# Performance work log

Measured on AMD Instinct MI355X. Metric: run time of the kernel, lower is better.

Reference implementation:

```python
import jax, jax.numpy as jnp
import numpy as np

B, S, HID = 1, 2048, 4096
NH, NKV, HD = 32, 8, 128
GROUPS = NH // NKV
SCALING = HD ** -0.5


def approx_matmul(a, b):
    # BaselineApproxMatmulFP16: matmul performed in fp16 precision
    return jnp.matmul(a.astype(jnp.float16), b.astype(jnp.float16)).astype(a.dtype)


def rotate_half(x):
    x1, x2 = jnp.split(x, 2, axis=-1)
    return jnp.concatenate([-x2, x1], axis=-1)


def setup_inputs() -> dict:
    key = jax.random.key(0)
    ks = jax.random.split(key, 6)
    hidden_states = jax.random.normal(ks[0], (B, S, HID), jnp.float32)
    # Proper RoPE tables (HF llama convention: freqs duplicated across halves)
    inv_freq = 1.0 / (10000.0 ** (jnp.arange(0, HD, 2, dtype=jnp.float32) / HD))
    t = jnp.arange(S, dtype=jnp.float32)
    freqs = jnp.outer(t, inv_freq)                      # [S, HD/2]
    emb = jnp.concatenate([freqs, freqs], axis=-1)      # [S, HD]
    cos = jnp.cos(emb)[None]                            # [B, S, HD]
    sin = jnp.sin(emb)[None]
    # Additive causal mask [B,1,S,S]
    causal = jnp.triu(jnp.full((S, S), -1e9, jnp.float32), k=1)[None, None]
    scale = 0.02
    wq = jax.random.normal(ks[1], (HID, NH * HD), jnp.float32) * scale
    wk = jax.random.normal(ks[2], (HID, NKV * HD), jnp.float32) * scale
    wv = jax.random.normal(ks[3], (HID, NKV * HD), jnp.float32) * scale
    wo = jax.random.normal(ks[4], (NH * HD, HID), jnp.float32) * scale
    return {"hidden_states": hidden_states, "cos": cos, "sin": sin,
            "attn_mask": causal, "wq": wq, "wk": wk, "wv": wv, "wo": wo}


def reference(hidden_states, cos, sin, attn_mask, wq, wk, wv, wo):
    x = hidden_states
    # projections -> [B, heads, S, HD]
    q = (x @ wq).reshape(B, S, NH, HD).transpose(0, 2, 1, 3)
    k = (x @ wk).reshape(B, S, NKV, HD).transpose(0, 2, 1, 3)
    v = (x @ wv).reshape(B, S, NKV, HD).transpose(0, 2, 1, 3)
    # RoPE
    c = cos[:, None]  # [B,1,S,HD]
    s = sin[:, None]
    q = q * c + rotate_half(q) * s
    k = k * c + rotate_half(k) * s
    # repeat_kv (GQA): [B,NKV,S,HD] -> [B,NH,S,HD]
    k = jnp.repeat(k, GROUPS, axis=1)
    v = jnp.repeat(v, GROUPS, axis=1)
    # eager attention with fp16 approx matmul
    attn = approx_matmul(q, k.transpose(0, 1, 3, 2)) * SCALING  # [B,NH,S,S]
    attn = attn + attn_mask
    attn = jax.nn.softmax(attn.astype(jnp.float32), axis=-1).astype(q.dtype)
    out = approx_matmul(attn, v)                                # [B,NH,S,HD]
    out = out.transpose(0, 2, 1, 3).reshape(B, S, NH * HD)
    return out @ wo
```

## Files before the change

kernel.cpp:

```cpp
#include <hip/hip_runtime.h>
#include <hip/hip_bf16.h>
#include <hip/hip_fp16.h>

typedef _Float16 half8 __attribute__((ext_vector_type(8)));
typedef _Float16 half4 __attribute__((ext_vector_type(4)));
typedef float f32x4 __attribute__((ext_vector_type(4)));
typedef unsigned int u32;

#define S_LEN 2048
#define HID_DIM 4096
#define N_HEADS 32
#define N_KV 8
#define HEAD_DIM 128
#define SCALE_QK 0.08838834764831845f

__device__ __forceinline__ void async16(void* lds, const void* gptr) {
  __builtin_amdgcn_global_load_lds(
      (const __attribute__((address_space(1))) u32*)gptr,
      (__attribute__((address_space(3))) u32*)lds, 16, 0, 0);
}

__device__ __forceinline__ void transpose_tile(const float* __restrict__ src,
                                               _Float16* __restrict__ dst, int R, int C,
                                               int bx, int by, float (*tile)[73], int t) {
  {
    const int c4 = (t & 15) * 4;
    const int r0 = t >> 4;
#pragma unroll
    for (int i = 0; i < 4; i++) {
      int r = r0 + 16 * i;
      float4 v = *(const float4*)&src[(long)(by * 64 + r) * C + bx * 64 + c4];
      tile[r][c4] = v.x; tile[r][c4 + 1] = v.y; tile[r][c4 + 2] = v.z; tile[r][c4 + 3] = v.w;
    }
  }
  __syncthreads();
  const int kc = t & 7;
  const int n0 = t >> 3;
#pragma unroll
  for (int p = 0; p < 2; p++) {
    int n = n0 + 32 * p;
    half8 o;
#pragma unroll
    for (int j = 0; j < 8; j++) o[j] = (_Float16)tile[kc * 8 + j][n];
    *(half8*)&dst[(long)(bx * 64 + n) * R + by * 64 + kc * 8] = o;
  }
}

__global__ void prep_kernel(const float* __restrict__ x, _Float16* __restrict__ Xh,
                            const float* __restrict__ wq, _Float16* __restrict__ WqT,
                            const float* __restrict__ wk, const float* __restrict__ wv,
                            _Float16* __restrict__ WkvT) {
  __shared__ float tile[64][73];
  const int bid = blockIdx.x;
  const int t = threadIdx.x;
  if (bid < 4096) {
    int i = bid * 256 + t;
    float4 a = ((const float4*)x)[2 * i];
    float4 b = ((const float4*)x)[2 * i + 1];
    half8 h;
    h[0] = (_Float16)a.x; h[1] = (_Float16)a.y; h[2] = (_Float16)a.z; h[3] = (_Float16)a.w;
    h[4] = (_Float16)b.x; h[5] = (_Float16)b.y; h[6] = (_Float16)b.z; h[7] = (_Float16)b.w;
    ((half8*)Xh)[i] = h;
  } else if (bid < 8192) {
    int tt = bid - 4096;
    transpose_tile(wq, WqT, 4096, 4096, tt & 63, tt >> 6, tile, t);
  } else if (bid < 9216) {
    int tt = bid - 8192;
    transpose_tile(wk, WkvT, 4096, 1024, tt & 15, tt >> 4, tile, t);
  } else {
    int tt = bid - 9216;
    transpose_tile(wv, WkvT + (size_t)1024 * 4096, 4096, 1024, tt & 15, tt >> 4, tile, t);
  }
}

__global__ __launch_bounds__(256, 3) void gemm_qkv(
    const _Float16* __restrict__ A, const _Float16* __restrict__ BtQ,
    const _Float16* __restrict__ BtKV, _Float16* __restrict__ Qt,
    _Float16* __restrict__ Kt, _Float16* __restrict__ Vt,
    const float* __restrict__ cosb, const float* __restrict__ sinb) {
  __shared__ __align__(16) char smem[34816];
  _Float16* As = (_Float16*)smem;
  _Float16* Bs = (_Float16*)(smem + 16384);
  const int K = 4096;
  const int tid = threadIdx.x, lane = tid & 63, wid = tid >> 6;
  const int row0 = blockIdx.y * 128;
  const int col0 = blockIdx.x * 128;
  const int wm = wid >> 1, wn = wid & 1;
  const int lr = lane & 15, lg = lane >> 4;

  const _Float16* bbase = (col0 < 4096) ? (BtQ + (long)col0 * K)
                                        : (BtKV + (long)(col0 - 4096) * K);
  const int scol = ((lane & 7) ^ ((lane >> 3) & 7)) * 8;
  const _Float16* aptr = A + (long)(row0 + wid * 32 + (lane >> 3)) * K + scol;
  const _Float16* bptr = bbase + (long)(wid * 32 + (lane >> 3)) * K + scol;
  _Float16* alds = As + (wid * 4) * 512;
  _Float16* blds = Bs + (wid * 4) * 512;

  f32x4 acc[4][4] = {};
  for (int k0 = 0; k0 < K; k0 += 64) {
#pragma unroll
    for (int j = 0; j < 4; j++) {
      async16(alds + j * 512, aptr + k0 + (long)j * 8 * K);
      async16(blds + j * 512, bptr + k0 + (long)j * 8 * K);
    }
    __syncthreads();
    half8 a[2][4], b[2][4];
#pragma unroll
    for (int kk = 0; kk < 2; kk++)
#pragma unroll
      for (int mf = 0; mf < 4; mf++) {
        a[kk][mf] = *(const half8*)&As[(wm * 64 + mf * 16 + lr) * 64 +
                                       (((kk * 4 + lg) ^ (lr & 7)) * 8)];
        b[kk][mf] = *(const half8*)&Bs[(wn * 64 + mf * 16 + lr) * 64 +
                                       (((kk * 4 + lg) ^ (lr & 7)) * 8)];
      }
#pragma unroll
    for (int kk = 0; kk < 2; kk++)
#pragma unroll
      for (int mf = 0; mf < 4; mf++)
#pragma unroll
        for (int nf = 0; nf < 4; nf++)
          acc[mf][nf] =
              __builtin_amdgcn_mfma_f32_16x16x32_f16(a[kk][mf], b[kk][nf], acc[mf][nf], 0, 0, 0);
    __syncthreads();
  }

  if (col0 < 4096) {
#pragma unroll
    for (int mf = 0; mf < 4; mf++)
#pragma unroll
      for (int nf = 0; nf < 4; nf++) {
        int rbase = row0 + wm * 64 + mf * 16 + lg * 4;
        int col = col0 + wn * 64 + nf * 16 + lr;
        int h = col >> 7, d = col & 127;
        long off = ((long)((h * 128 + (rbase >> 4)) * 4 + (d >> 5))) * 512 +
                   ((d >> 3) & 3) * 128 + (rbase & 15) * 8 + (d & 7);
#pragma unroll
        for (int i = 0; i < 4; i++) Qt[off + i * 8] = (_Float16)acc[mf][nf][i];
      }
  } else if (col0 < 5120) {
    const int g = (col0 - 4096) >> 7;
    float* fl = (float*)smem;
    if (wn == 1) {
#pragma unroll
      for (int mf = 0; mf < 4; mf++)
#pragma unroll
        for (int nf = 0; nf < 4; nf++)
#pragma unroll
          for (int i = 0; i < 4; i++)
            fl[(wm * 64 + mf * 16 + lg * 4 + i) * 68 + nf * 16 + lr] = acc[mf][nf][i];
    }
    __syncthreads();
    if (wn == 0) {
#pragma unroll
      for (int mf = 0; mf < 4; mf++)
#pragma unroll
        for (int nf = 0; nf < 4; nf++)
#pragma unroll
          for (int i = 0; i < 4; i++) {
            int s_local = wm * 64 + mf * 16 + lg * 4 + i;
            int d = nf * 16 + lr;
            int s_glob = row0 + s_local;
            float lo = acc[mf][nf][i];
            float hi = fl[s_local * 68 + d];
            float c = cosb[s_glob * 128 + d];
            float sn = sinb[s_glob * 128 + d];
            long off = ((long)((g * 128 + (s_glob >> 4)) * 4 + (d >> 5))) * 512 +
                       ((d >> 3) & 3) * 128 + (s_glob & 15) * 8 + (d & 7);
            Kt[off] = (_Float16)(lo * c - hi * sn);
            Kt[off + 1024] = (_Float16)(hi * c + lo * sn);
          }
    }
  } else {
#pragma unroll
    for (int mf = 0; mf < 4; mf++)
#pragma unroll
      for (int nf = 0; nf < 4; nf++) {
        int rbase = row0 + wm * 64 + mf * 16 + lg * 4;
        int col = col0 + wn * 64 + nf * 16 + lr;
        int gc = col - 5120;
        int gq = gc >> 7, d = gc & 127;
        int dt = d >> 4, lrr = d & 15;
        int kvb = rbase >> 5, lgv = (rbase >> 3) & 3, j = rbase & 7;
        half4 v;
#pragma unroll
        for (int i = 0; i < 4; i++) v[i] = (_Float16)acc[mf][nf][i];
        long off = ((long)(gq * 64 + kvb) * 8 + dt) * 512 + (lgv * 16 + lrr) * 8 + j;
        *(half4*)&Vt[off] = v;
      }
  }
}

__global__ __launch_bounds__(256, 3) void gemm_out(
    const _Float16* __restrict__ A, const _Float16* __restrict__ Bt,
    float* __restrict__ C) {
  __shared__ _Float16 As[128 * 64];
  __shared__ _Float16 Bs[128 * 64];
  const int K = 4096;
  const int tid = threadIdx.x, lane = tid & 63, wid = tid >> 6;
  const int row0 = blockIdx.y * 128;
  const int col0 = blockIdx.x * 128;
  const int wm = wid >> 1, wn = wid & 1;
  const int lr = lane & 15, lg = lane >> 4;

  const int scol = ((lane & 7) ^ ((lane >> 3) & 7)) * 8;
  const _Float16* aptr = A + (long)(row0 + wid * 32 + (lane >> 3)) * K + scol;
  const _Float16* bptr = Bt + (long)(col0 + wid * 32 + (lane >> 3)) * K + scol;
  _Float16* alds = As + (wid * 4) * 512;
  _Float16* blds = Bs + (wid * 4) * 512;

  f32x4 acc[4][4] = {};
  for (int k0 = 0; k0 < K; k0 += 64) {
#pragma unroll
    for (int j = 0; j < 4; j++) {
      async16(alds + j * 512, aptr + k0 + (long)j * 8 * K);
      async16(blds + j * 512, bptr + k0 + (long)j * 8 * K);
    }
    __syncthreads();
    half8 a[2][4], b[2][4];
#pragma unroll
    for (int kk = 0; kk < 2; kk++)
#pragma unroll
      for (int mf = 0; mf < 4; mf++) {
        a[kk][mf] = *(const half8*)&As[(wm * 64 + mf * 16 + lr) * 64 +
                                       (((kk * 4 + lg) ^ (lr & 7)) * 8)];
        b[kk][mf] = *(const half8*)&Bs[(wn * 64 + mf * 16 + lr) * 64 +
                                       (((kk * 4 + lg) ^ (lr & 7)) * 8)];
      }
#pragma unroll
    for (int kk = 0; kk < 2; kk++)
#pragma unroll
      for (int mf = 0; mf < 4; mf++)
#pragma unroll
        for (int nf = 0; nf < 4; nf++)
          acc[mf][nf] =
              __builtin_amdgcn_mfma_f32_16x16x32_f16(a[kk][mf], b[kk][nf], acc[mf][nf], 0, 0, 0);
    __syncthreads();
  }
#pragma unroll
  for (int mf = 0; mf < 4; mf++)
#pragma unroll
    for (int nf = 0; nf < 4; nf++) {
      int rbase = row0 + wm * 64 + mf * 16 + lg * 4;
      int col = col0 + wn * 64 + nf * 16 + lr;
#pragma unroll
      for (int i = 0; i < 4; i++)
        C[(long)(rbase + i) * 4096 + col] = acc[mf][nf][i];
    }
}

__global__ __launch_bounds__(256, 3) void attn_wo_kernel(
    const _Float16* __restrict__ Qt, const _Float16* __restrict__ Kt,
    const _Float16* __restrict__ Vt, _Float16* __restrict__ O,
    const float* __restrict__ cosb, const float* __restrict__ sinb,
    const float* __restrict__ wo, _Float16* __restrict__ WoT) {
  __shared__ __align__(16) char smem[36864];
  const int tid = threadIdx.x;
  const int bid = blockIdx.x;

  if (bid >= 1024) {
    int tt = bid - 1024;
    transpose_tile(wo, WoT, 4096, 4096, tt & 63, tt >> 6, (float(*)[73])smem, tid);
    return;
  }

  _Float16* Kb = (_Float16*)smem;
  _Float16* Vb = (_Float16*)(smem + 16384);
  _Float16* Pb = (_Float16*)(smem + 32768) + (tid >> 6) * 512;

  const int lane = tid & 63;
  const int wid = tid >> 6;
  const int g = bid & 7;
  const int qidx = bid >> 3;
  const int qt16 = (qidx < 64) ? (2 * qidx) : (2 * (127 - qidx) + 1);
  const int h = g * 4 + wid;
  const int qrow0 = qt16 * 16;
  const int ntiles = (qrow0 + 47) >> 5;
  const int lr = lane & 15;
  const int lg = lane >> 4;

  half8 qf[4];
  {
    const _Float16* qp = Qt + ((long)(h * 128 + qt16) * 4) * 512 + lane * 8;
#pragma unroll
    for (int t = 0; t < 4; t++) qf[t] = *(const half8*)(qp + t * 512);
    int s = qrow0 + lr;
#pragma unroll
    for (int t = 0; t < 2; t++) {
      const float* cp = cosb + s * 128 + t * 32 + lg * 8;
      const float* sp = sinb + s * 128 + t * 32 + lg * 8;
#pragma unroll
      for (int j = 0; j < 8; j++) {
        float c = cp[j], sn = sp[j];
        float lo = (float)qf[t][j], hi = (float)qf[t + 2][j];
        qf[t][j]     = (_Float16)(lo * c - hi * sn);
        qf[t + 2][j] = (_Float16)(hi * c + lo * sn);
      }
    }
  }

  const _Float16* kgb = Kt + (long)g * 128 * 2048 + lane * 8;
  const _Float16* vgb = Vt + (long)g * 64 * 4096 + lane * 8;

  {
    async16(&Kb[(2 * wid) * 512], kgb + (2 * wid) * 512);
    async16(&Kb[(2 * wid + 1) * 512], kgb + (2 * wid + 1) * 512);
    async16(&Vb[(2 * wid) * 512], vgb + (2 * wid) * 512);
    async16(&Vb[(2 * wid + 1) * 512], vgb + (2 * wid + 1) * 512);
  }
  __syncthreads();

  f32x4 oacc[8] = {};
  float mrow[4] = {-1e30f, -1e30f, -1e30f, -1e30f};
  float lsum[4] = {0.f, 0.f, 0.f, 0.f};

  for (int t = 0; t < ntiles; t++) {
    const int kb = t * 32;
    const int cur = t & 1;
    if (t + 1 < ntiles) {
      const _Float16* ks = kgb + (long)(t + 1) * 4096;
      const _Float16* vs = vgb + (long)(t + 1) * 4096;
      async16(&Kb[(cur ^ 1) * 4096 + (2 * wid) * 512], ks + (2 * wid) * 512);
      async16(&Kb[(cur ^ 1) * 4096 + (2 * wid + 1) * 512], ks + (2 * wid + 1) * 512);
      async16(&Vb[(cur ^ 1) * 4096 + (2 * wid) * 512], vs + (2 * wid) * 512);
      async16(&Vb[(cur ^ 1) * 4096 + (2 * wid + 1) * 512], vs + (2 * wid + 1) * 512);
    }

    half8 kf[8];
#pragma unroll
    for (int c = 0; c < 8; c++)
      kf[c] = *(const half8*)&Kb[cur * 4096 + c * 512 + lane * 8];
    half8 vf[8];
#pragma unroll
    for (int dt = 0; dt < 8; dt++)
      vf[dt] = *(const half8*)&Vb[cur * 4096 + dt * 512 + lane * 8];

    f32x4 sacc[2] = {};
    __builtin_amdgcn_s_setprio(1);
#pragma unroll
    for (int s = 0; s < 2; s++)
#pragma unroll
      for (int t2 = 0; t2 < 4; t2++)
        sacc[s] = __builtin_amdgcn_mfma_f32_16x16x32_f16(qf[t2], kf[s * 4 + t2], sacc[s], 0, 0, 0);
    __builtin_amdgcn_s_setprio(0);

#pragma unroll
    for (int i = 0; i < 4; i++) {
      sacc[0][i] *= SCALE_QK;
      sacc[1][i] *= SCALE_QK;
    }
    if (t == ntiles - 1) {
#pragma unroll
      for (int i = 0; i < 4; i++) {
        int qrow = qrow0 + lg * 4 + i;
        if (kb + lr > qrow) sacc[0][i] = -1e30f;
        if (kb + 16 + lr > qrow) sacc[1][i] = -1e30f;
      }
    }
    float mx[4];
    bool grow = false;
#pragma unroll
    for (int i = 0; i < 4; i++) {
      mx[i] = fmaxf(sacc[0][i], sacc[1][i]);
      grow |= (mx[i] > mrow[i] + 4.0f);
    }
    if (__any((int)grow)) {
#pragma unroll
      for (int i = 0; i < 4; i++) {
        float m = mx[i];
        m = fmaxf(m, __shfl_xor(m, 1));
        m = fmaxf(m, __shfl_xor(m, 2));
        m = fmaxf(m, __shfl_xor(m, 4));
        m = fmaxf(m, __shfl_xor(m, 8));
        float mn = fmaxf(mrow[i], m);
        float scl = __expf(mrow[i] - mn);
        mrow[i] = mn;
        lsum[i] *= scl;
#pragma unroll
        for (int dt = 0; dt < 8; dt++) oacc[dt][i] *= scl;
      }
    }
    float p[2][4];
#pragma unroll
    for (int i = 0; i < 4; i++) {
      p[0][i] = __expf(sacc[0][i] - mrow[i]);
      p[1][i] = __expf(sacc[1][i] - mrow[i]);
      lsum[i] += p[0][i] + p[1][i];
    }

#pragma unroll
    for (int sub = 0; sub < 2; sub++)
#pragma unroll
      for (int i = 0; i < 4; i++)
        Pb[(lg * 4 + i) * 32 + sub * 16 + lr] = (_Float16)p[sub][i];
    half8 pa = *(const half8*)&Pb[lr * 32 + lg * 8];

    __builtin_amdgcn_s_setprio(1);
#pragma unroll
    for (int dt = 0; dt < 8; dt++)
      oacc[dt] = __builtin_amdgcn_mfma_f32_16x16x32_f16(pa, vf[dt], oacc[dt], 0, 0, 0);
    __builtin_amdgcn_s_setprio(0);

    __syncthreads();
  }

#pragma unroll
  for (int i = 0; i < 4; i++) {
    float t2 = lsum[i];
    t2 += __shfl_xor(t2, 1);
    t2 += __shfl_xor(t2, 2);
    t2 += __shfl_xor(t2, 4);
    t2 += __shfl_xor(t2, 8);
    lsum[i] = t2;
  }
#pragma unroll
  for (int dt = 0; dt < 8; dt++) {
#pragma unroll
    for (int i = 0; i < 4; i++) {
      float o = oacc[dt][i] / lsum[i];
      O[(long)(qrow0 + lg * 4 + i) * HID_DIM + h * HEAD_DIM + dt * 16 + lr] = (_Float16)o;
    }
  }
}

extern "C" void kernel_launch(void* const* d_in, const int* in_sizes, int n_in,
                              void* d_out, int out_size, void* d_ws, size_t ws_size,
                              hipStream_t stream) {
  const float* x    = (const float*)d_in[0];
  const float* cosb = (const float*)d_in[1];
  const float* sinb = (const float*)d_in[2];
  const float* wq = (const float*)d_in[4];
  const float* wk = (const float*)d_in[5];
  const float* wv = (const float*)d_in[6];
  const float* wo = (const float*)d_in[7];
  float* out = (float*)d_out;

  char* ws = (char*)d_ws;
  _Float16* Xh    = (_Float16*)(ws);
  _Float16* Oattn = Xh;
  _Float16* Qt    = (_Float16*)(ws + (size_t)(16 << 20));
  _Float16* Kt    = (_Float16*)(ws + (size_t)(32 << 20));
  _Float16* Vt    = (_Float16*)(ws + (size_t)(36 << 20));
  _Float16* WqT   = (_Float16*)(ws + (size_t)(40 << 20));
  _Float16* WoT   = WqT;
  _Float16* WkvT  = (_Float16*)d_out;

  dim3 b256(256);

  prep_kernel<<<dim3(10240), b256, 0, stream>>>(x, Xh, wq, WqT, wk, wv, WkvT);

  gemm_qkv<<<dim3(6144 / 128, S_LEN / 128), b256, 0, stream>>>(Xh, WqT, WkvT, Qt, Kt, Vt,
                                                               cosb, sinb);

  attn_wo_kernel<<<dim3(1024 + 4096), b256, 0, stream>>>(Qt, Kt, Vt, Oattn, cosb, sinb, wo, WoT);

  gemm_out<<<dim3(4096 / 128, S_LEN / 128), b256, 0, stream>>>(Oattn, WoT, out);
}
```

Baseline: 290.9 us.

## Triple-buffer K/V tiles in attention and swizzle GEMM block order for L2 reuse

The attention kernel moves from a double-buffered K/V pipeline to a three-stage ring. Loads are issued two tiles ahead, explicit vmcnt/lgkmcnt waits and raw barriers replace the per-iteration __syncthreads, and the first loads are issued before the Q/RoPE setup. The QKV and output GEMMs remap block indices with a grouped swizzle so neighbouring blocks share A/B tiles in cache. Shared memory grows to about 52KB per attention block, which may reduce occupancy, and the hand-written vmcnt counts must match the number of outstanding loads.

```diff
diff --git a/kernel.cpp b/kernel.cpp
--- a/kernel.cpp
+++ b/kernel.cpp
@@ -83,8 +83,10 @@
   _Float16* Bs = (_Float16*)(smem + 16384);
   const int K = 4096;
   const int tid = threadIdx.x, lane = tid & 63, wid = tid >> 6;
-  const int row0 = blockIdx.y * 128;
-  const int col0 = blockIdx.x * 128;
+  const int lin = blockIdx.y * 48 + blockIdx.x;
+  const int swz = (lin & 7) * 96 + (lin >> 3);
+  const int row0 = (swz / 48) * 128;
+  const int col0 = (swz % 48) * 128;
   const int wm = wid >> 1, wn = wid & 1;
   const int lr = lane & 15, lg = lane >> 4;
 
@@ -198,8 +200,10 @@
   __shared__ _Float16 Bs[128 * 64];
   const int K = 4096;
   const int tid = threadIdx.x, lane = tid & 63, wid = tid >> 6;
-  const int row0 = blockIdx.y * 128;
-  const int col0 = blockIdx.x * 128;
+  const int lin = blockIdx.y * 32 + blockIdx.x;
+  const int swz = (lin & 7) * 64 + (lin >> 3);
+  const int row0 = (swz / 32) * 128;
+  const int col0 = (swz % 32) * 128;
   const int wm = wid >> 1, wn = wid & 1;
   const int lr = lane & 15, lg = lane >> 4;
 
@@ -254,7 +258,7 @@
     const _Float16* __restrict__ Vt, _Float16* __restrict__ O,
     const float* __restrict__ cosb, const float* __restrict__ sinb,
     const float* __restrict__ wo, _Float16* __restrict__ WoT) {
-  __shared__ __align__(16) char smem[36864];
+  __shared__ __align__(16) char smem[53248];
   const int tid = threadIdx.x;
   const int bid = blockIdx.x;
 
@@ -265,8 +269,8 @@
   }
 
   _Float16* Kb = (_Float16*)smem;
-  _Float16* Vb = (_Float16*)(smem + 16384);
-  _Float16* Pb = (_Float16*)(smem + 32768) + (tid >> 6) * 512;
+  _Float16* Vb = (_Float16*)(smem + 24576);
+  _Float16* Pb = (_Float16*)(smem + 49152) + (tid >> 6) * 512;
 
   const int lane = tid & 63;
   const int wid = tid >> 6;
@@ -279,6 +283,24 @@
   const int lr = lane & 15;
   const int lg = lane >> 4;
 
+  const _Float16* kgb = Kt + (long)g * 128 * 2048 + lane * 8;
+  const _Float16* vgb = Vt + (long)g * 64 * 4096 + lane * 8;
+
+  {
+    async16(&Kb[(2 * wid) * 512], kgb + (2 * wid) * 512);
+    async16(&Kb[(2 * wid + 1) * 512], kgb + (2 * wid + 1) * 512);
+    async16(&Vb[(2 * wid) * 512], vgb + (2 * wid) * 512);
+    async16(&Vb[(2 * wid + 1) * 512], vgb + (2 * wid + 1) * 512);
+    if (ntiles > 1) {
+      const _Float16* ks = kgb + 4096;
+      const _Float16* vs = vgb + 4096;
+      async16(&Kb[4096 + (2 * wid) * 512], ks + (2 * wid) * 512);
+      async16(&Kb[4096 + (2 * wid + 1) * 512], ks + (2 * wid + 1) * 512);
+      async16(&Vb[4096 + (2 * wid) * 512], vs + (2 * wid) * 512);
+      async16(&Vb[4096 + (2 * wid + 1) * 512], vs + (2 * wid + 1) * 512);
+    }
+  }
+
   half8 qf[4];
   {
     const _Float16* qp = Qt + ((long)(h * 128 + qt16) * 4) * 512 + lane * 8;
@@ -299,32 +321,21 @@
     }
   }
 
-  const _Float16* kgb = Kt + (long)g * 128 * 2048 + lane * 8;
-  const _Float16* vgb = Vt + (long)g * 64 * 4096 + lane * 8;
-
-  {
-    async16(&Kb[(2 * wid) * 512], kgb + (2 * wid) * 512);
-    async16(&Kb[(2 * wid + 1) * 512], kgb + (2 * wid + 1) * 512);
-    async16(&Vb[(2 * wid) * 512], vgb + (2 * wid) * 512);
-    async16(&Vb[(2 * wid + 1) * 512], vgb + (2 * wid + 1) * 512);
-  }
-  __syncthreads();
-
   f32x4 oacc[8] = {};
   float mrow[4] = {-1e30f, -1e30f, -1e30f, -1e30f};
   float lsum[4] = {0.f, 0.f, 0.f, 0.f};
 
   for (int t = 0; t < ntiles; t++) {
     const int kb = t * 32;
-    const int cur = t & 1;
+    const int cur = t % 3;
     if (t + 1 < ntiles) {
-      const _Float16* ks = kgb + (long)(t + 1) * 4096;
-      const _Float16* vs = vgb + (long)(t + 1) * 4096;
-      async16(&Kb[(cur ^ 1) * 4096 + (2 * wid) * 512], ks + (2 * wid) * 512);
-      async16(&Kb[(cur ^ 1) * 4096 + (2 * wid + 1) * 512], ks + (2 * wid + 1) * 512);
-      async16(&Vb[(cur ^ 1) * 4096 + (2 * wid) * 512], vs + (2 * wid) * 512);
-      async16(&Vb[(cur ^ 1) * 4096 + (2 * wid + 1) * 512], vs + (2 * wid + 1) * 512);
-    }
+      asm volatile("s_waitcnt vmcnt(4)" ::: "memory");
+    } else {
+      asm volatile("s_waitcnt vmcnt(0)" ::: "memory");
+    }
+    __builtin_amdgcn_sched_barrier(0);
+    __builtin_amdgcn_s_barrier();
+    __builtin_amdgcn_sched_barrier(0);
 
     half8 kf[8];
 #pragma unroll
@@ -334,6 +345,20 @@
 #pragma unroll
     for (int dt = 0; dt < 8; dt++)
       vf[dt] = *(const half8*)&Vb[cur * 4096 + dt * 512 + lane * 8];
+    asm volatile("s_waitcnt lgkmcnt(0)" ::: "memory");
+    __builtin_amdgcn_sched_barrier(0);
+    __builtin_amdgcn_s_barrier();
+    __builtin_amdgcn_sched_barrier(0);
+
+    if (t + 2 < ntiles) {
+      const int nxt = (t + 2) % 3;
+      const _Float16* ks = kgb + (long)(t + 2) * 4096;
+      const _Float16* vs = vgb + (long)(t + 2) * 4096;
+      async16(&Kb[nxt * 4096 + (2 * wid) * 512], ks + (2 * wid) * 512);
+      async16(&Kb[nxt * 4096 + (2 * wid + 1) * 512], ks + (2 * wid + 1) * 512);
+      async16(&Vb[nxt * 4096 + (2 * wid) * 512], vs + (2 * wid) * 512);
+      async16(&Vb[nxt * 4096 + (2 * wid + 1) * 512], vs + (2 * wid + 1) * 512);
+    }
 
     f32x4 sacc[2] = {};
     __builtin_amdgcn_s_setprio(1);
@@ -400,8 +425,6 @@
     for (int dt = 0; dt < 8; dt++)
       oacc[dt] = __builtin_amdgcn_mfma_f32_16x16x32_f16(pa, vf[dt], oacc[dt], 0, 0, 0);
     __builtin_amdgcn_s_setprio(0);
-
-    __syncthreads();
   }
 
 #pragma unroll
```

New measurement: 301.1 us. +3.5%, slower.

## Rewrite QKV GEMM as 256x256 tile, 8-wave double-buffered pipelined kernel

Applied to the files above, without the earlier changes.

Replaces the 128x128, 4-wave QKV projection GEMM with a 256x256 tile, 512-thread kernel that uses 128KB of LDS, double-buffered with async global-to-LDS loads. Loads for the next K-step are interleaved with MFMA phases using explicit barriers, sched_barrier pins and setprio. The aim is more data reuse per block and hiding of memory latency behind compute. In exchange, only 192 blocks are launched and LDS use per block is high, which limits occupancy and may underfill the CUs.

```diff
diff --git a/kernel.cpp b/kernel.cpp
--- a/kernel.cpp
+++ b/kernel.cpp
@@ -19,6 +19,8 @@
       (const __attribute__((address_space(1))) u32*)gptr,
       (__attribute__((address_space(3))) u32*)lds, 16, 0, 0);
 }
+
+#define PIN() __builtin_amdgcn_sched_barrier(0)
 
 __device__ __forceinline__ void transpose_tile(const float* __restrict__ src,
                                                _Float16* __restrict__ dst, int R, int C,
@@ -73,64 +75,127 @@
   }
 }
 
-__global__ __launch_bounds__(256, 3) void gemm_qkv(
+__global__ __launch_bounds__(512, 2) void gemm_qkv8(
     const _Float16* __restrict__ A, const _Float16* __restrict__ BtQ,
     const _Float16* __restrict__ BtKV, _Float16* __restrict__ Qt,
     _Float16* __restrict__ Kt, _Float16* __restrict__ Vt,
     const float* __restrict__ cosb, const float* __restrict__ sinb) {
-  __shared__ __align__(16) char smem[34816];
-  _Float16* As = (_Float16*)smem;
-  _Float16* Bs = (_Float16*)(smem + 16384);
+  __shared__ __align__(16) char smem[131072];
   const int K = 4096;
-  const int tid = threadIdx.x, lane = tid & 63, wid = tid >> 6;
-  const int row0 = blockIdx.y * 128;
-  const int col0 = blockIdx.x * 128;
-  const int wm = wid >> 1, wn = wid & 1;
+  const int NT = 64;
+  const int tid = threadIdx.x, lane = tid & 63, w = tid >> 6;
+  const int row0 = blockIdx.y * 256;
+  const int col0 = blockIdx.x * 256;
+  const int wm = w >> 2, wn = w & 3;
   const int lr = lane & 15, lg = lane >> 4;
 
   const _Float16* bbase = (col0 < 4096) ? (BtQ + (long)col0 * K)
                                         : (BtKV + (long)(col0 - 4096) * K);
-  const int scol = ((lane & 7) ^ ((lane >> 3) & 7)) * 8;
-  const _Float16* aptr = A + (long)(row0 + wid * 32 + (lane >> 3)) * K + scol;
-  const _Float16* bptr = bbase + (long)(wid * 32 + (lane >> 3)) * K + scol;
-  _Float16* alds = As + (wid * 4) * 512;
-  _Float16* blds = Bs + (wid * 4) * 512;
-
-  f32x4 acc[4][4] = {};
-  for (int k0 = 0; k0 < K; k0 += 64) {
-#pragma unroll
-    for (int j = 0; j < 4; j++) {
-      async16(alds + j * 512, aptr + k0 + (long)j * 8 * K);
-      async16(blds + j * 512, bptr + k0 + (long)j * 8 * K);
-    }
-    __syncthreads();
-    half8 a[2][4], b[2][4];
-#pragma unroll
-    for (int kk = 0; kk < 2; kk++)
-#pragma unroll
-      for (int mf = 0; mf < 4; mf++) {
-        a[kk][mf] = *(const half8*)&As[(wm * 64 + mf * 16 + lr) * 64 +
-                                       (((kk * 4 + lg) ^ (lr & 7)) * 8)];
-        b[kk][mf] = *(const half8*)&Bs[(wn * 64 + mf * 16 + lr) * 64 +
-                                       (((kk * 4 + lg) ^ (lr & 7)) * 8)];
-      }
-#pragma unroll
-    for (int kk = 0; kk < 2; kk++)
-#pragma unroll
-      for (int mf = 0; mf < 4; mf++)
-#pragma unroll
-        for (int nf = 0; nf < 4; nf++)
-          acc[mf][nf] =
-              __builtin_amdgcn_mfma_f32_16x16x32_f16(a[kk][mf], b[kk][nf], acc[mf][nf], 0, 0, 0);
-    __syncthreads();
+  const int srow = lane >> 3;
+  const int schunk = (lane & 7) ^ ((lane & 32) ? 2 : 0);
+  const _Float16* aS0 = A + (long)(row0 + (2 * w) * 8 + srow) * K + schunk * 8;
+  const _Float16* aS1 = A + (long)(row0 + (2 * w + 1) * 8 + srow) * K + schunk * 8;
+  const _Float16* bS0 = bbase + (long)((2 * w) * 8 + srow) * K + schunk * 8;
+  const _Float16* bS1 = bbase + (long)((2 * w + 1) * 8 + srow) * K + schunk * 8;
+  char* AsB = smem;
+  char* BsB = smem + 65536;
+  const long HSTEP = (long)128 * K;
+
+#define STG_A(sl, h, t) do { \
+    async16(AsB + (sl) * 32768 + (h) * 16384 + (2 * w) * 1024,     aS0 + (h) * HSTEP + (t) * 64); \
+    async16(AsB + (sl) * 32768 + (h) * 16384 + (2 * w + 1) * 1024, aS1 + (h) * HSTEP + (t) * 64); \
+  } while (0)
+#define STG_B(sl, h, t) do { \
+    async16(BsB + (sl) * 32768 + (h) * 16384 + (2 * w) * 1024,     bS0 + (h) * HSTEP + (t) * 64); \
+    async16(BsB + (sl) * 32768 + (h) * 16384 + (2 * w + 1) * 1024, bS1 + (h) * HSTEP + (t) * 64); \
+  } while (0)
+
+  const int cs0 = ((0 + lg) ^ ((lr & 4) ? 2 : 0)) * 8;
+  const int cs1 = ((4 + lg) ^ ((lr & 4) ? 2 : 0)) * 8;
+  const _Float16* Af = (const _Float16*)AsB + wm * 8192 + lr * 64;
+  const _Float16* Bf = (const _Float16*)BsB + (wn >> 1) * 8192 + ((wn & 1) * 64 + lr) * 64;
+
+  f32x4 acc[8][4] = {};
+
+  STG_A(0, 0, 0); STG_A(0, 1, 0); STG_B(0, 0, 0); STG_B(0, 1, 0);
+  STG_A(1, 0, 1);
+  asm volatile("s_waitcnt vmcnt(2)" ::: "memory");
+  PIN(); __builtin_amdgcn_s_barrier(); PIN();
+
+  for (int t = 0; t < NT; ++t) {
+    const int sl = t & 1;
+    const int so = sl * 16384;
+    half8 bf[4], af[4];
+
+#pragma unroll
+    for (int nf = 0; nf < 4; nf++) bf[nf] = *(const half8*)(Bf + so + nf * 1024 + cs0);
+#pragma unroll
+    for (int m = 0; m < 4; m++) af[m] = *(const half8*)(Af + so + m * 1024 + cs0);
+    if (t + 1 < NT) STG_A(sl ^ 1, 1, t + 1);
+    PIN(); __builtin_amdgcn_s_barrier(); PIN();
+    __builtin_amdgcn_s_setprio(1);
+#pragma unroll
+    for (int m = 0; m < 4; m++)
+#pragma unroll
+      for (int nf = 0; nf < 4; nf++)
+        acc[m][nf] = __builtin_amdgcn_mfma_f32_16x16x32_f16(af[m], bf[nf], acc[m][nf], 0, 0, 0);
+    __builtin_amdgcn_s_setprio(0);
+    PIN(); __builtin_amdgcn_s_barrier(); PIN();
+
+#pragma unroll
+    for (int m = 0; m < 4; m++) af[m] = *(const half8*)(Af + so + (4 + m) * 1024 + cs0);
+    if (t + 1 < NT) STG_B(sl ^ 1, 0, t + 1);
+    PIN(); __builtin_amdgcn_s_barrier(); PIN();
+    __builtin_amdgcn_s_setprio(1);
+#pragma unroll
+    for (int m = 0; m < 4; m++)
+#pragma unroll
+      for (int nf = 0; nf < 4; nf++)
+        acc[4 + m][nf] = __builtin_amdgcn_mfma_f32_16x16x32_f16(af[m], bf[nf], acc[4 + m][nf], 0, 0, 0);
+    __builtin_amdgcn_s_setprio(0);
+    PIN(); __builtin_amdgcn_s_barrier(); PIN();
+
+#pragma unroll
+    for (int nf = 0; nf < 4; nf++) bf[nf] = *(const half8*)(Bf + so + nf * 1024 + cs1);
+#pragma unroll
+    for (int m = 0; m < 4; m++) af[m] = *(const half8*)(Af + so + m * 1024 + cs1);
+    if (t + 1 < NT) STG_B(sl ^ 1, 1, t + 1);
+    PIN(); __builtin_amdgcn_s_barrier(); PIN();
+    __builtin_amdgcn_s_setprio(1);
+#pragma unroll
+    for (int m = 0; m < 4; m++)
+#pragma unroll
+      for (int nf = 0; nf < 4; nf++)
+        acc[m][nf] = __builtin_amdgcn_mfma_f32_16x16x32_f16(af[m], bf[nf], acc[m][nf], 0, 0, 0);
+    __builtin_amdgcn_s_setprio(0);
+    PIN(); __builtin_amdgcn_s_barrier(); PIN();
+
+#pragma unroll
+    for (int m = 0; m < 4; m++) af[m] = *(const half8*)(Af + so + (4 + m) * 1024 + cs1);
+    PIN(); __builtin_amdgcn_s_barrier(); PIN();
+    __builtin_amdgcn_s_setprio(1);
+#pragma unroll
+    for (int m = 0; m < 4; m++)
+#pragma unroll
+      for (int nf = 0; nf < 4; nf++)
+        acc[4 + m][nf] = __builtin_amdgcn_mfma_f32_16x16x32_f16(af[m], bf[nf], acc[4 + m][nf], 0, 0, 0);
+    __builtin_amdgcn_s_setprio(0);
+    PIN(); __builtin_amdgcn_s_barrier(); PIN();
+    if (t + 2 < NT) {
+      STG_A(sl, 0, t + 2);
+      asm volatile("s_waitcnt vmcnt(2)" ::: "memory");
+    } else if (t + 1 < NT) {
+      asm volatile("s_waitcnt vmcnt(0)" ::: "memory");
+    }
+    PIN(); __builtin_amdgcn_s_barrier(); PIN();
   }
 
   if (col0 < 4096) {
 #pragma unroll
-    for (int mf = 0; mf < 4; mf++)
+    for (int mf = 0; mf < 8; mf++)
 #pragma unroll
       for (int nf = 0; nf < 4; nf++) {
-        int rbase = row0 + wm * 64 + mf * 16 + lg * 4;
+        int rbase = row0 + wm * 128 + mf * 16 + lg * 4;
         int col = col0 + wn * 64 + nf * 16 + lr;
         int h = col >> 7, d = col & 127;
         long off = ((long)((h * 128 + (rbase >> 4)) * 4 + (d >> 5))) * 512 +
@@ -139,30 +204,31 @@
         for (int i = 0; i < 4; i++) Qt[off + i * 8] = (_Float16)acc[mf][nf][i];
       }
   } else if (col0 < 5120) {
-    const int g = (col0 - 4096) >> 7;
     float* fl = (float*)smem;
-    if (wn == 1) {
-#pragma unroll
-      for (int mf = 0; mf < 4; mf++)
+    float* myreg = fl + (wm * 2 + (wn >> 1)) * 8192;
+    if (wn & 1) {
+#pragma unroll
+      for (int mf = 0; mf < 8; mf++)
 #pragma unroll
         for (int nf = 0; nf < 4; nf++)
 #pragma unroll
           for (int i = 0; i < 4; i++)
-            fl[(wm * 64 + mf * 16 + lg * 4 + i) * 68 + nf * 16 + lr] = acc[mf][nf][i];
+            myreg[(mf * 16 + lg * 4 + i) * 64 + nf * 16 + lr] = acc[mf][nf][i];
     }
     __syncthreads();
-    if (wn == 0) {
-#pragma unroll
-      for (int mf = 0; mf < 4; mf++)
+    if (!(wn & 1)) {
+      const int g = ((col0 - 4096) >> 7) + (wn >> 1);
+#pragma unroll
+      for (int mf = 0; mf < 8; mf++)
 #pragma unroll
         for (int nf = 0; nf < 4; nf++)
 #pragma unroll
           for (int i = 0; i < 4; i++) {
-            int s_local = wm * 64 + mf * 16 + lg * 4 + i;
+            int rl = mf * 16 + lg * 4 + i;
             int d = nf * 16 + lr;
-            int s_glob = row0 + s_local;
+            int s_glob = row0 + wm * 128 + rl;
             float lo = acc[mf][nf][i];
-            float hi = fl[s_local * 68 + d];
+            float hi = myreg[rl * 64 + d];
             float c = cosb[s_glob * 128 + d];
             float sn = sinb[s_glob * 128 + d];
             long off = ((long)((g * 128 + (s_glob >> 4)) * 4 + (d >> 5))) * 512 +
@@ -173,10 +239,10 @@
     }
   } else {
 #pragma unroll
-    for (int mf = 0; mf < 4; mf++)
+    for (int mf = 0; mf < 8; mf++)
 #pragma unroll
       for (int nf = 0; nf < 4; nf++) {
-        int rbase = row0 + wm * 64 + mf * 16 + lg * 4;
+        int rbase = row0 + wm * 128 + mf * 16 + lg * 4;
         int col = col0 + wn * 64 + nf * 16 + lr;
         int gc = col - 5120;
         int gq = gc >> 7, d = gc & 127;
@@ -189,6 +255,8 @@
         *(half4*)&Vt[off] = v;
       }
   }
+#undef STG_A
+#undef STG_B
 }
 
 __global__ __launch_bounds__(256, 3) void gemm_out(
@@ -449,8 +517,8 @@
 
   prep_kernel<<<dim3(10240), b256, 0, stream>>>(x, Xh, wq, WqT, wk, wv, WkvT);
 
-  gemm_qkv<<<dim3(6144 / 128, S_LEN / 128), b256, 0, stream>>>(Xh, WqT, WkvT, Qt, Kt, Vt,
-                                                               cosb, sinb);
+  gemm_qkv8<<<dim3(6144 / 256, S_LEN / 256), dim3(512), 0, stream>>>(
+      Xh, WqT, WkvT, Qt, Kt, Vt, cosb, sinb);
 
   attn_wo_kernel<<<dim3(1024 + 4096), b256, 0, stream>>>(Qt, Kt, Vt, Oattn, cosb, sinb, wo, WoT);
 
```

Result: slower. 300.6 us (+3.3%).
